# Performance work log

Measured on AMD Instinct MI355X. Metric: run time of the kernel, lower is better.

Reference implementation:

```python
import jax, jax.numpy as jnp
import numpy as np


def gcn_layer(x, W, b, src, dst):
    """PyG GCNConv with improved=True: A_hat = A + 2I, D^-1/2 A_hat D^-1/2 X W + b."""
    n = x.shape[0]
    xw = x @ W  # [N, H]
    # degree counts each incoming edge (weight 1) plus self-loop weight 2
    deg = jnp.zeros((n,), x.dtype).at[dst].add(jnp.ones((src.shape[0],), x.dtype)) + 2.0
    dinv = jax.lax.rsqrt(deg)  # deg >= 2 always
    norm = (dinv[src] * dinv[dst])[:, None]  # [E, 1]
    agg = jax.ops.segment_sum(xw[src] * norm, dst, num_segments=n)  # scatter-add to dst
    agg = agg + (2.0 * dinv * dinv)[:, None] * xw  # self-loop contribution (weight 2)
    return agg + b


def xavier(k, shape):
    lim = (6.0 / (shape[0] + shape[1])) ** 0.5
    return jax.random.uniform(k, shape, jnp.float32, -lim, lim)


def setup_inputs() -> dict:
    key = jax.random.key(0)
    ks = jax.random.split(key, 8)
    N, E, D = 100_000, 1_600_000, 64  # nodes, edges, features_dim
    H1, H2 = 64, 64                   # gnn_dims
    M1, M2 = 128, 64                  # ind_pol_dims
    rep = jax.random.normal(ks[0], (N, D), jnp.float32)
    edge_index = jax.random.randint(ks[1], (2, E), 0, N, jnp.int32)
    return {
        "rep": rep,
        "edge_index": edge_index,
        "W1": xavier(ks[2], (D, H1)), "b1": jnp.zeros((H1,), jnp.float32),
        "W2": xavier(ks[3], (H1, H2)), "b2": jnp.zeros((H2,), jnp.float32),
        "Wa": xavier(ks[4], (H2 + D, M1)), "ba": jnp.zeros((M1,), jnp.float32),
        "Wb": xavier(ks[5], (M1, M2)), "bb": jnp.zeros((M2,), jnp.float32),
        "Wo": xavier(ks[6], (M2, 1)), "bo": jnp.zeros((1,), jnp.float32),
    }


def reference(rep, edge_index, W1, b1, W2, b2, Wa, ba, Wb, bb, Wo, bo):
    src, dst = edge_index[0], edge_index[1]
    # eval mode: f.dropout(training=False) is identity
    h = jax.nn.relu(gcn_layer(rep, W1, b1, src, dst))
    h = jax.nn.relu(gcn_layer(h, W2, b2, src, dst))
    z = jnp.concatenate([rep, h], axis=1)  # [N, D + H2]
    z = jax.nn.relu(z @ Wa + ba)
    z = jax.nn.relu(z @ Wb + bb)
    prob = jax.nn.sigmoid(z @ Wo + bo)[:, 0]  # [N]
    # gumbel_softmax(hard=True, tau=1) over logits = [1-p, p] (torch semantics:
    # probabilities fed directly as logits, as in the original code)
    logits = jnp.stack([1.0 - prob, prob], axis=1)  # [N, 2]
    u = jax.random.uniform(jax.random.key(42), logits.shape, jnp.float32, 1e-20, 1.0)
    g = -jnp.log(-jnp.log(u))
    y = jax.nn.softmax(logits + g, axis=1)
    hard = jax.nn.one_hot(jnp.argmax(y, axis=1), 2, dtype=y.dtype)
    st = hard + y - jax.lax.stop_gradient(y)  # straight-through
    ind = st @ jnp.array([[0.0], [1.0]], dtype=y.dtype)  # mm with [[0],[1]]
    return (prob, ind[:, 0])
```

## Files before the change

kernel.cpp:

```cpp
#include <hip/hip_runtime.h>
#include <math.h>


__device__ __forceinline__ unsigned rotl32(unsigned x, int r) {
  return (x << r) | (x >> (32 - r));
}

__device__ __forceinline__ void threefry2x32(unsigned k0, unsigned k1,
                                             unsigned x0, unsigned x1,
                                             unsigned& o0, unsigned& o1) {
  unsigned ks2 = k0 ^ k1 ^ 0x1BD11BDAu;
#define TF_RND(r) { x0 += x1; x1 = rotl32(x1, (r)); x1 ^= x0; }
  x0 += k0; x1 += k1;
  TF_RND(13) TF_RND(15) TF_RND(26) TF_RND(6)
  x0 += k1; x1 += ks2 + 1u;
  TF_RND(17) TF_RND(29) TF_RND(16) TF_RND(24)
  x0 += ks2; x1 += k0 + 2u;
  TF_RND(13) TF_RND(15) TF_RND(26) TF_RND(6)
  x0 += k0; x1 += k1 + 3u;
  TF_RND(17) TF_RND(29) TF_RND(16) TF_RND(24)
  x0 += k1; x1 += ks2 + 4u;
  TF_RND(13) TF_RND(15) TF_RND(26) TF_RND(6)
  x0 += ks2; x1 += k0 + 5u;
#undef TF_RND
  o0 = x0; o1 = x1;
}

__device__ __forceinline__ unsigned jax_random_bits_u32(unsigned k0, unsigned k1,
                                                        unsigned flat_idx) {
  unsigned a, b;
  threefry2x32(k0, k1, 0u, flat_idx, a, b);
  return a ^ b;
}

#define BSHIFT 8
#define BMASK 255

__global__ __launch_bounds__(256) void coarse_hist_kernel(
    const int* __restrict__ dst, int* __restrict__ coarse, int E) {
  __shared__ int h[512];
  for (int i = threadIdx.x; i < 512; i += 256) h[i] = 0;
  __syncthreads();
  for (int e = blockIdx.x * blockDim.x + threadIdx.x; e < E;
       e += gridDim.x * blockDim.x)
    atomicAdd(&h[dst[e] >> BSHIFT], 1);
  __syncthreads();
  for (int i = threadIdx.x; i < 512; i += 256)
    if (h[i]) atomicAdd(&coarse[i], h[i]);
}

__global__ __launch_bounds__(512) void coarse_scan_kernel(
    const int* __restrict__ coarse, int* __restrict__ bbase,
    int* __restrict__ cbase, int NBUCK) {
  __shared__ int sh[512];
  int t = threadIdx.x;
  int v = (t < NBUCK) ? coarse[t] : 0;
  sh[t] = v;
  __syncthreads();
  for (int o = 1; o < 512; o <<= 1) {
    int a = (t >= o) ? sh[t - o] : 0;
    __syncthreads();
    sh[t] += a;
    __syncthreads();
  }
  if (t < NBUCK) {
    int ex = sh[t] - v;
    bbase[t] = ex;
    cbase[t] = ex;
    if (t == NBUCK - 1) bbase[NBUCK] = sh[t];
  }
}

#define CHUNK 4096
__global__ __launch_bounds__(256) void bucket_scatter_kernel(
    const int* __restrict__ src, const int* __restrict__ dst,
    int* __restrict__ cbase, int* __restrict__ pkB, int E) {
  __shared__ int sS[CHUNK];
  __shared__ int dS[CHUNK];
  __shared__ int cnt[512];
  __shared__ int base[512];
  const int t = threadIdx.x;
  const int e0 = blockIdx.x * CHUNK;
  const int n = min(CHUNK, E - e0);
  for (int i = t; i < 512; i += 256) cnt[i] = 0;
  for (int i = t; i < n; i += 256) {
    sS[i] = src[e0 + i];
    dS[i] = dst[e0 + i];
  }
  __syncthreads();
  for (int i = t; i < n; i += 256) atomicAdd(&cnt[dS[i] >> BSHIFT], 1);
  __syncthreads();
  for (int i = t; i < 512; i += 256) {
    int c = cnt[i];
    base[i] = c ? atomicAdd(&cbase[i], c) : 0;
  }
  __syncthreads();
  for (int i = t; i < 512; i += 256) cnt[i] = 0;
  __syncthreads();
  for (int i = t; i < n; i += 256) {
    int d = dS[i];
    int b = d >> BSHIFT;
    int r = atomicAdd(&cnt[b], 1);
    pkB[base[b] + r] = ((d & BMASK) << 20) | sS[i];
  }
}

__global__ __launch_bounds__(256) void bucket_finalize_kernel(
    const int* __restrict__ pkB, const int* __restrict__ bbase,
    int* __restrict__ off, float* __restrict__ dinv, int* __restrict__ srcS,
    int N) {
  __shared__ int cnt[256];
  __shared__ int sh[256];
  const int t = threadIdx.x;
  const int b = blockIdx.x;
  const int lo = bbase[b], hi = bbase[b + 1];
  cnt[t] = 0;
  __syncthreads();
  for (int i = lo + t; i < hi; i += 256) atomicAdd(&cnt[pkB[i] >> 20], 1);
  __syncthreads();
  const int deg = cnt[t];
  sh[t] = deg;
  __syncthreads();
  for (int o = 1; o < 256; o <<= 1) {
    int a = (t >= o) ? sh[t - o] : 0;
    __syncthreads();
    sh[t] += a;
    __syncthreads();
  }
  const int ex = sh[t] - deg;
  const int node = (b << BSHIFT) + t;
  if (node < N) {
    off[node] = lo + ex;
    dinv[node] = 1.0f / sqrtf((float)deg + 2.0f);
    if (node == N - 1) off[N] = hi;
  }
  cnt[t] = lo + ex;
  __syncthreads();
  for (int i = lo + t; i < hi; i += 256) {
    int u = pkB[i];
    int pos = atomicAdd(&cnt[u >> 20], 1);
    srcS[pos] = u & 0xFFFFF;
  }
}

__global__ __launch_bounds__(256) void aggregate_kernel(
    const float* __restrict__ xws, const int* __restrict__ srcS,
    const int* __restrict__ off, const float* __restrict__ dinv,
    const float* __restrict__ bias, float* __restrict__ h, int N) {
  int node = (blockIdx.x * blockDim.x + threadIdx.x) >> 6;
  int lane = threadIdx.x & 63;
  int g = lane >> 4;
  int fq = lane & 15;
  if (node >= N) return;
  const float4* xw4 = (const float4*)xws;
  int beg = off[node], end = off[node + 1];
  float4 a0 = make_float4(0.f, 0.f, 0.f, 0.f);
  float4 a1 = a0, a2 = a0, a3 = a0;
  for (int e = beg; e < end; e += 16) {
    int e0 = e + g, e1 = e + 4 + g, e2 = e + 8 + g, e3 = e + 12 + g;
    int s0 = srcS[min(e0, end - 1)];
    int s1 = srcS[min(e1, end - 1)];
    int s2 = srcS[min(e2, end - 1)];
    int s3 = srcS[min(e3, end - 1)];
    float4 v0 = xw4[(size_t)s0 * 16 + fq];
    float4 v1 = xw4[(size_t)s1 * 16 + fq];
    float4 v2 = xw4[(size_t)s2 * 16 + fq];
    float4 v3 = xw4[(size_t)s3 * 16 + fq];
    if (e0 < end) { a0.x += v0.x; a0.y += v0.y; a0.z += v0.z; a0.w += v0.w; }
    if (e1 < end) { a1.x += v1.x; a1.y += v1.y; a1.z += v1.z; a1.w += v1.w; }
    if (e2 < end) { a2.x += v2.x; a2.y += v2.y; a2.z += v2.z; a2.w += v2.w; }
    if (e3 < end) { a3.x += v3.x; a3.y += v3.y; a3.z += v3.z; a3.w += v3.w; }
  }
  float4 a;
  a.x = (a0.x + a1.x) + (a2.x + a3.x);
  a.y = (a0.y + a1.y) + (a2.y + a3.y);
  a.z = (a0.z + a1.z) + (a2.z + a3.z);
  a.w = (a0.w + a1.w) + (a2.w + a3.w);
  a.x += __shfl_xor(a.x, 16, 64); a.x += __shfl_xor(a.x, 32, 64);
  a.y += __shfl_xor(a.y, 16, 64); a.y += __shfl_xor(a.y, 32, 64);
  a.z += __shfl_xor(a.z, 16, 64); a.z += __shfl_xor(a.z, 32, 64);
  a.w += __shfl_xor(a.w, 16, 64); a.w += __shfl_xor(a.w, 32, 64);
  if (g == 0) {
    float di = dinv[node];
    float4 self = xw4[(size_t)node * 16 + fq];
    float4 b = ((const float4*)bias)[fq];
    float4 r;
    r.x = fmaxf(di * (a.x + 2.0f * self.x) + b.x, 0.f);
    r.y = fmaxf(di * (a.y + 2.0f * self.y) + b.y, 0.f);
    r.z = fmaxf(di * (a.z + 2.0f * self.z) + b.z, 0.f);
    r.w = fmaxf(di * (a.w + 2.0f * self.w) + b.w, 0.f);
    *(float4*)&h[(size_t)node * 64 + fq * 4] = r;
  }
}

__global__ __launch_bounds__(256) void gemm64v2_kernel(
    const float* __restrict__ X, const float* __restrict__ W,
    const float* __restrict__ dinv, float* __restrict__ Y, int N, int flags) {
  __shared__ float Ws[64 * 64];
  __shared__ float Xs[64 * 68];
  const int t = threadIdx.x;
  {
    const float4* W4 = (const float4*)W;
    float4* Ws4 = (float4*)Ws;
    for (int i = t; i < 16 * 64; i += 256) Ws4[i] = W4[i];
  }
  const int row0 = blockIdx.x * 64;
  for (int i = t; i < 64 * 16; i += 256) {
    int r = i >> 4, c4 = i & 15;
    int gr = row0 + r;
    float4 v = make_float4(0.f, 0.f, 0.f, 0.f);
    if (gr < N) v = *(const float4*)&X[(size_t)gr * 64 + c4 * 4];
    *(float4*)&Xs[r * 68 + c4 * 4] = v;
  }
  __syncthreads();

  const int tx = t & 15, ty = t >> 4;
  const int c0 = tx * 4;
  const int r0 = ty * 4;
  float acc[4][4];
#pragma unroll
  for (int i = 0; i < 4; ++i)
#pragma unroll
    for (int j = 0; j < 4; ++j) acc[i][j] = 0.f;

#pragma unroll 4
  for (int k4 = 0; k4 < 16; ++k4) {
    float4 xv[4];
#pragma unroll
    for (int i = 0; i < 4; ++i)
      xv[i] = *(const float4*)&Xs[(r0 + i) * 68 + k4 * 4];
#pragma unroll
    for (int kk = 0; kk < 4; ++kk) {
      float w[4];
#pragma unroll
      for (int j = 0; j < 4; ++j) w[j] = Ws[(k4 * 4 + kk) * 64 + c0 + j];
      const float xk[4] = {
          kk == 0 ? xv[0].x : kk == 1 ? xv[0].y : kk == 2 ? xv[0].z : xv[0].w,
          kk == 0 ? xv[1].x : kk == 1 ? xv[1].y : kk == 2 ? xv[1].z : xv[1].w,
          kk == 0 ? xv[2].x : kk == 1 ? xv[2].y : kk == 2 ? xv[2].z : xv[2].w,
          kk == 0 ? xv[3].x : kk == 1 ? xv[3].y : kk == 2 ? xv[3].z : xv[3].w};
#pragma unroll
      for (int i = 0; i < 4; ++i)
#pragma unroll
        for (int j = 0; j < 4; ++j) acc[i][j] = fmaf(xk[i], w[j], acc[i][j]);
    }
  }

#pragma unroll
  for (int i = 0; i < 4; ++i) {
    int gr = row0 + r0 + i;
    if (gr >= N) continue;
    float sc = (flags & 8) ? dinv[gr] : 1.0f;
    float4 v = make_float4(acc[i][0], acc[i][1], acc[i][2], acc[i][3]);
    if (flags & 8) { v.x *= sc; v.y *= sc; v.z *= sc; v.w *= sc; }
    *(float4*)&Y[(size_t)gr * 64 + c0] = v;
  }
}

__global__ __launch_bounds__(256) void head_mega_kernel(
    const float* __restrict__ rep, const float* __restrict__ h2,
    const float* __restrict__ Wa, const float* __restrict__ ba,
    const float* __restrict__ Wb, const float* __restrict__ bb,
    const float* __restrict__ Wo, const float* __restrict__ bo,
    float* __restrict__ out, int N) {
  __shared__ float Xs[64 * 128];
  __shared__ float Wbuf[32 * 128];
  const int t = threadIdx.x;
  const int row0 = blockIdx.x * 64;

  for (int i = t; i < 2048; i += 256) {
    int r = i >> 5, c4 = i & 31;
    int gr = row0 + r;
    float4 v = make_float4(0.f, 0.f, 0.f, 0.f);
    if (gr < N)
      v = (c4 < 16) ? *(const float4*)&rep[(size_t)gr * 64 + c4 * 4]
                    : *(const float4*)&h2[(size_t)gr * 64 + (c4 - 16) * 4];
    int scol = (c4 * 4 + ((r >> 2) << 2)) & 127;
    *(float4*)&Xs[r * 128 + scol] = v;
  }

  const int tx = t & 15, ty = t >> 4;
  const int cL = tx * 4;
  const int cH = 64 + tx * 4;
  const int r0 = ty * 4;
  float za[4][8];
#pragma unroll
  for (int i = 0; i < 4; ++i)
#pragma unroll
    for (int j = 0; j < 8; ++j) za[i][j] = 0.f;

  for (int chunk = 0; chunk < 4; ++chunk) {
    __syncthreads();
    const float4* Wa4 = (const float4*)(Wa + chunk * 32 * 128);
    float4* Wd = (float4*)Wbuf;
    for (int i = t; i < 1024; i += 256) Wd[i] = Wa4[i];
    __syncthreads();
    const int kb = chunk * 32;
#pragma unroll 2
    for (int kk = 0; kk < 32; ++kk) {
      const int kc = (kb + kk + (ty << 2)) & 127;
      float x[4];
#pragma unroll
      for (int i = 0; i < 4; ++i) x[i] = Xs[(r0 + i) * 128 + kc];
      float4 w0 = *(const float4*)&Wbuf[kk * 128 + cL];
      float4 w1 = *(const float4*)&Wbuf[kk * 128 + cH];
      const float w[8] = {w0.x, w0.y, w0.z, w0.w, w1.x, w1.y, w1.z, w1.w};
#pragma unroll
      for (int i = 0; i < 4; ++i)
#pragma unroll
        for (int j = 0; j < 8; ++j) za[i][j] = fmaf(x[i], w[j], za[i][j]);
    }
  }
#pragma unroll
  for (int i = 0; i < 4; ++i) {
#pragma unroll
    for (int j = 0; j < 4; ++j) {
      za[i][j] = fmaxf(za[i][j] + ba[cL + j], 0.f);
      za[i][4 + j] = fmaxf(za[i][4 + j] + ba[cH + j], 0.f);
    }
  }

  __syncthreads();
  float* zaS = Xs;
  {
    int sL = (cL + (ty << 2)) & 127;
    int sH = (cH + (ty << 2)) & 127;
#pragma unroll
    for (int i = 0; i < 4; ++i) {
      *(float4*)&zaS[(r0 + i) * 128 + sL] =
          make_float4(za[i][0], za[i][1], za[i][2], za[i][3]);
      *(float4*)&zaS[(r0 + i) * 128 + sH] =
          make_float4(za[i][4], za[i][5], za[i][6], za[i][7]);
    }
  }

  const int c0b = tx * 4;
  float zb[4][4];
#pragma unroll
  for (int i = 0; i < 4; ++i)
#pragma unroll
    for (int j = 0; j < 4; ++j) zb[i][j] = 0.f;

  for (int chunk = 0; chunk < 2; ++chunk) {
    __syncthreads();
    const float4* Wb4 = (const float4*)(Wb + chunk * 64 * 64);
    float4* Wd = (float4*)Wbuf;
    for (int i = t; i < 1024; i += 256) Wd[i] = Wb4[i];
    __syncthreads();
    const int kb = chunk * 64;
#pragma unroll 4
    for (int kk = 0; kk < 64; ++kk) {
      const int kc = (kb + kk + (ty << 2)) & 127;
      float x[4];
#pragma unroll
      for (int i = 0; i < 4; ++i) x[i] = zaS[(r0 + i) * 128 + kc];
      float4 w = *(const float4*)&Wbuf[kk * 64 + c0b];
      const float wj[4] = {w.x, w.y, w.z, w.w};
#pragma unroll
      for (int i = 0; i < 4; ++i)
#pragma unroll
        for (int j = 0; j < 4; ++j) zb[i][j] = fmaf(x[i], wj[j], zb[i][j]);
    }
  }
  float part[4];
#pragma unroll
  for (int i = 0; i < 4; ++i) {
    part[i] = 0.f;
#pragma unroll
    for (int j = 0; j < 4; ++j) {
      float v = fmaxf(zb[i][j] + bb[c0b + j], 0.f);
      part[i] = fmaf(v, Wo[c0b + j], part[i]);
    }
  }
  __syncthreads();
  float* red = Wbuf;
#pragma unroll
  for (int i = 0; i < 4; ++i) red[tx * 68 + r0 + i] = part[i];
  __syncthreads();
  if (t < 64) {
    int gr = row0 + t;
    if (gr < N) {
      float s = 0.f;
#pragma unroll
      for (int u = 0; u < 16; ++u) s += red[u * 68 + t];
      float w = s + bo[0];
      float p = 1.0f / (1.0f + expf(-w));
      unsigned i = (unsigned)gr;
      unsigned bits0 = jax_random_bits_u32(0u, 42u, 2u * i);
      unsigned bits1 = jax_random_bits_u32(0u, 42u, 2u * i + 1u);
      float f0 = __uint_as_float((bits0 >> 9) | 0x3f800000u) - 1.0f;
      float f1 = __uint_as_float((bits1 >> 9) | 0x3f800000u) - 1.0f;
      float u0 = fmaxf(1e-20f, f0 + 1e-20f);
      float u1 = fmaxf(1e-20f, f1 + 1e-20f);
      float g0 = -logf(-logf(u0));
      float g1 = -logf(-logf(u1));
      float a0 = (1.0f - p) + g0;
      float a1 = p + g1;
      float m = fmaxf(a0, a1);
      float e0 = expf(a0 - m), e1 = expf(a1 - m);
      float ssum = e0 + e1;
      float y0 = e0 / ssum, y1 = e1 / ssum;
      float hard1 = (y1 > y0) ? 1.0f : 0.0f;
      float st1 = (hard1 + y1) - y1;
      out[gr] = p;
      out[N + gr] = st1;
    }
  }
}

extern "C" void kernel_launch(void* const* d_in, const int* in_sizes, int n_in,
                              void* d_out, int out_size, void* d_ws, size_t ws_size,
                              hipStream_t stream) {
  const float* rep = (const float*)d_in[0];
  const int* ei = (const int*)d_in[1];
  const float* W1 = (const float*)d_in[2];
  const float* b1 = (const float*)d_in[3];
  const float* W2 = (const float*)d_in[4];
  const float* b2 = (const float*)d_in[5];
  const float* Wa = (const float*)d_in[6];
  const float* ba = (const float*)d_in[7];
  const float* Wb = (const float*)d_in[8];
  const float* bb = (const float*)d_in[9];
  const float* Wo = (const float*)d_in[10];
  const float* bo = (const float*)d_in[11];
  float* out = (float*)d_out;

  const int N = in_sizes[0] / 64;
  const int E = in_sizes[1] / 2;
  const int* srcI = ei;
  const int* dstI = ei + E;

  const int NBUCK = (N + 255) >> BSHIFT;

  float* ws = (float*)d_ws;
  float* bufA = ws;
  float* bufB = bufA + (size_t)N * 64;
  float* dinv = bufB + (size_t)N * 64;
  int* coarse = (int*)(dinv + N);
  int* bbase = coarse + 512;
  int* cbase = bbase + 513;
  int* off = cbase + 512;
  int* pkB = off + N + 1;
  int* srcS = pkB + E;

  const int nb64 = (N + 63) / 64;
  const int nbW = (N + 3) / 4;
  const int nbA = (E + CHUNK - 1) / CHUNK;

  hipMemsetAsync(coarse, 0, 512 * 4, stream);
  coarse_hist_kernel<<<256, 256, 0, stream>>>(dstI, coarse, E);
  coarse_scan_kernel<<<1, 512, 0, stream>>>(coarse, bbase, cbase, NBUCK);
  bucket_scatter_kernel<<<nbA, 256, 0, stream>>>(srcI, dstI, cbase, pkB, E);
  bucket_finalize_kernel<<<NBUCK, 256, 0, stream>>>(pkB, bbase, off, dinv,
                                                    srcS, N);

  gemm64v2_kernel<<<nb64, 256, 0, stream>>>(rep, W1, dinv, bufA, N, 8);
  aggregate_kernel<<<nbW, 256, 0, stream>>>(bufA, srcS, off, dinv, b1, bufB, N);

  gemm64v2_kernel<<<nb64, 256, 0, stream>>>(bufB, W2, dinv, bufA, N, 8);
  aggregate_kernel<<<nbW, 256, 0, stream>>>(bufA, srcS, off, dinv, b2, bufB, N);

  head_mega_kernel<<<nb64, 256, 0, stream>>>(rep, bufB, Wa, ba, Wb, bb, Wo, bo,
                                             out, N);
}
```

Measured before the change: 391.0 us.

## Fuse neighbor aggregation into following GEMM and MLP head kernels

Each aggregation is fused into its consumer. The first layer's gather now feeds a 64-row tile in shared memory that is multiplied by W2 in the same kernel, and the second layer's gather fills the h2 half of the head kernel's input tile. This removes two intermediate N×64 writes and reads and two kernel launches. The gather now runs over 64-node blocks, 16 nodes per wave, with fewer blocks in flight, which may reduce latency hiding for the irregular gathers. The head inner loops are also reworked to load float4 activations from shared memory.

```diff
diff --git a/kernel.cpp b/kernel.cpp
--- a/kernel.cpp
+++ b/kernel.cpp
@@ -143,17 +143,10 @@
   }
 }
 
-__global__ __launch_bounds__(256) void aggregate_kernel(
-    const float* __restrict__ xws, const int* __restrict__ srcS,
-    const int* __restrict__ off, const float* __restrict__ dinv,
-    const float* __restrict__ bias, float* __restrict__ h, int N) {
-  int node = (blockIdx.x * blockDim.x + threadIdx.x) >> 6;
-  int lane = threadIdx.x & 63;
-  int g = lane >> 4;
-  int fq = lane & 15;
-  if (node >= N) return;
-  const float4* xw4 = (const float4*)xws;
-  int beg = off[node], end = off[node + 1];
+__device__ __forceinline__ float4 gather_node_row(
+    const float4* __restrict__ xw4, const int* __restrict__ srcS,
+    const float* __restrict__ dinv, const float* __restrict__ bias,
+    int node, int beg, int end, int g, int fq) {
   float4 a0 = make_float4(0.f, 0.f, 0.f, 0.f);
   float4 a1 = a0, a2 = a0, a3 = a0;
   for (int e = beg; e < end; e += 16) {
@@ -180,22 +173,20 @@
   a.y += __shfl_xor(a.y, 16, 64); a.y += __shfl_xor(a.y, 32, 64);
   a.z += __shfl_xor(a.z, 16, 64); a.z += __shfl_xor(a.z, 32, 64);
   a.w += __shfl_xor(a.w, 16, 64); a.w += __shfl_xor(a.w, 32, 64);
-  if (g == 0) {
-    float di = dinv[node];
-    float4 self = xw4[(size_t)node * 16 + fq];
-    float4 b = ((const float4*)bias)[fq];
-    float4 r;
-    r.x = fmaxf(di * (a.x + 2.0f * self.x) + b.x, 0.f);
-    r.y = fmaxf(di * (a.y + 2.0f * self.y) + b.y, 0.f);
-    r.z = fmaxf(di * (a.z + 2.0f * self.z) + b.z, 0.f);
-    r.w = fmaxf(di * (a.w + 2.0f * self.w) + b.w, 0.f);
-    *(float4*)&h[(size_t)node * 64 + fq * 4] = r;
-  }
+  float di = dinv[node];
+  float4 self = xw4[(size_t)node * 16 + fq];
+  float4 b = ((const float4*)bias)[fq];
+  float4 r;
+  r.x = fmaxf(di * (a.x + 2.0f * self.x) + b.x, 0.f);
+  r.y = fmaxf(di * (a.y + 2.0f * self.y) + b.y, 0.f);
+  r.z = fmaxf(di * (a.z + 2.0f * self.z) + b.z, 0.f);
+  r.w = fmaxf(di * (a.w + 2.0f * self.w) + b.w, 0.f);
+  return r;
 }
 
 __global__ __launch_bounds__(256) void gemm64v2_kernel(
     const float* __restrict__ X, const float* __restrict__ W,
-    const float* __restrict__ dinv, float* __restrict__ Y, int N, int flags) {
+    const float* __restrict__ dinv, float* __restrict__ Y, int N) {
   __shared__ float Ws[64 * 64];
   __shared__ float Xs[64 * 68];
   const int t = threadIdx.x;
@@ -250,15 +241,87 @@
   for (int i = 0; i < 4; ++i) {
     int gr = row0 + r0 + i;
     if (gr >= N) continue;
-    float sc = (flags & 8) ? dinv[gr] : 1.0f;
-    float4 v = make_float4(acc[i][0], acc[i][1], acc[i][2], acc[i][3]);
-    if (flags & 8) { v.x *= sc; v.y *= sc; v.z *= sc; v.w *= sc; }
+    float sc = dinv[gr];
+    float4 v = make_float4(acc[i][0] * sc, acc[i][1] * sc, acc[i][2] * sc,
+                           acc[i][3] * sc);
     *(float4*)&Y[(size_t)gr * 64 + c0] = v;
   }
 }
 
-__global__ __launch_bounds__(256) void head_mega_kernel(
-    const float* __restrict__ rep, const float* __restrict__ h2,
+__global__ __launch_bounds__(256) void agg_gemm_kernel(
+    const float* __restrict__ xws, const int* __restrict__ srcS,
+    const int* __restrict__ off, const float* __restrict__ dinv,
+    const float* __restrict__ bias, const float* __restrict__ W,
+    float* __restrict__ Y, int N) {
+  __shared__ float Xs[64 * 68];
+  __shared__ float Ws[64 * 64];
+  const int t = threadIdx.x;
+  const int row0 = blockIdx.x * 64;
+  const int wave = t >> 6, lane = t & 63;
+  const int g = lane >> 4, fq = lane & 15;
+
+  {
+    const float4* W4 = (const float4*)W;
+    float4* Ws4 = (float4*)Ws;
+    for (int i = t; i < 1024; i += 256) Ws4[i] = W4[i];
+  }
+  const float4* xw4 = (const float4*)xws;
+  for (int idx = wave; idx < 64; idx += 4) {
+    int node = row0 + idx;
+    if (node >= N) continue;
+    int beg = off[node], end = off[node + 1];
+    float4 r = gather_node_row(xw4, srcS, dinv, bias, node, beg, end, g, fq);
+    if (g == 0) *(float4*)&Xs[idx * 68 + fq * 4] = r;
+  }
+  __syncthreads();
+
+  const int tx = t & 15, ty = t >> 4;
+  const int c0 = tx * 4;
+  const int r0 = ty * 4;
+  float acc[4][4];
+#pragma unroll
+  for (int i = 0; i < 4; ++i)
+#pragma unroll
+    for (int j = 0; j < 4; ++j) acc[i][j] = 0.f;
+
+#pragma unroll 4
+  for (int k4 = 0; k4 < 16; ++k4) {
+    float4 xv[4];
+#pragma unroll
+    for (int i = 0; i < 4; ++i)
+      xv[i] = *(const float4*)&Xs[(r0 + i) * 68 + k4 * 4];
+#pragma unroll
+    for (int kk = 0; kk < 4; ++kk) {
+      float w[4];
+#pragma unroll
+      for (int j = 0; j < 4; ++j) w[j] = Ws[(k4 * 4 + kk) * 64 + c0 + j];
+      const float xk[4] = {
+          kk == 0 ? xv[0].x : kk == 1 ? xv[0].y : kk == 2 ? xv[0].z : xv[0].w,
+          kk == 0 ? xv[1].x : kk == 1 ? xv[1].y : kk == 2 ? xv[1].z : xv[1].w,
+          kk == 0 ? xv[2].x : kk == 1 ? xv[2].y : kk == 2 ? xv[2].z : xv[2].w,
+          kk == 0 ? xv[3].x : kk == 1 ? xv[3].y : kk == 2 ? xv[3].z : xv[3].w};
+#pragma unroll
+      for (int i = 0; i < 4; ++i)
+#pragma unroll
+        for (int j = 0; j < 4; ++j) acc[i][j] = fmaf(xk[i], w[j], acc[i][j]);
+    }
+  }
+
+#pragma unroll
+  for (int i = 0; i < 4; ++i) {
+    int gr = row0 + r0 + i;
+    if (gr >= N) continue;
+    float sc = dinv[gr];
+    float4 v = make_float4(acc[i][0] * sc, acc[i][1] * sc, acc[i][2] * sc,
+                           acc[i][3] * sc);
+    *(float4*)&Y[(size_t)gr * 64 + c0] = v;
+  }
+}
+
+__global__ __launch_bounds__(256) void agg_head_kernel(
+    const float* __restrict__ xws2, const int* __restrict__ srcS,
+    const int* __restrict__ off, const float* __restrict__ dinv,
+    const float* __restrict__ b2, const float* __restrict__ rep,
     const float* __restrict__ Wa, const float* __restrict__ ba,
     const float* __restrict__ Wb, const float* __restrict__ bb,
     const float* __restrict__ Wo, const float* __restrict__ bo,
@@ -267,16 +330,27 @@
   __shared__ float Wbuf[32 * 128];
   const int t = threadIdx.x;
   const int row0 = blockIdx.x * 64;
-
-  for (int i = t; i < 2048; i += 256) {
-    int r = i >> 5, c4 = i & 31;
+  const int wave = t >> 6, lane = t & 63;
+  const int g = lane >> 4, fq = lane & 15;
+
+  for (int i = t; i < 1024; i += 256) {
+    int r = i >> 4, c4 = i & 15;
     int gr = row0 + r;
     float4 v = make_float4(0.f, 0.f, 0.f, 0.f);
-    if (gr < N)
-      v = (c4 < 16) ? *(const float4*)&rep[(size_t)gr * 64 + c4 * 4]
-                    : *(const float4*)&h2[(size_t)gr * 64 + (c4 - 16) * 4];
+    if (gr < N) v = *(const float4*)&rep[(size_t)gr * 64 + c4 * 4];
     int scol = (c4 * 4 + ((r >> 2) << 2)) & 127;
     *(float4*)&Xs[r * 128 + scol] = v;
+  }
+  const float4* xw4 = (const float4*)xws2;
+  for (int idx = wave; idx < 64; idx += 4) {
+    int node = row0 + idx;
+    if (node >= N) continue;
+    int beg = off[node], end = off[node + 1];
+    float4 r = gather_node_row(xw4, srcS, dinv, b2, node, beg, end, g, fq);
+    if (g == 0) {
+      int scol = ((64 + fq * 4) + ((idx >> 2) << 2)) & 127;
+      *(float4*)&Xs[idx * 128 + scol] = r;
+    }
   }
 
   const int tx = t & 15, ty = t >> 4;
@@ -296,19 +370,26 @@
     for (int i = t; i < 1024; i += 256) Wd[i] = Wa4[i];
     __syncthreads();
     const int kb = chunk * 32;
-#pragma unroll 2
-    for (int kk = 0; kk < 32; ++kk) {
-      const int kc = (kb + kk + (ty << 2)) & 127;
-      float x[4];
-#pragma unroll
-      for (int i = 0; i < 4; ++i) x[i] = Xs[(r0 + i) * 128 + kc];
-      float4 w0 = *(const float4*)&Wbuf[kk * 128 + cL];
-      float4 w1 = *(const float4*)&Wbuf[kk * 128 + cH];
-      const float w[8] = {w0.x, w0.y, w0.z, w0.w, w1.x, w1.y, w1.z, w1.w};
+    for (int k4 = 0; k4 < 8; ++k4) {
+      const int kc = (kb + k4 * 4 + (ty << 2)) & 127;
+      float4 xq[4];
 #pragma unroll
       for (int i = 0; i < 4; ++i)
-#pragma unroll
-        for (int j = 0; j < 8; ++j) za[i][j] = fmaf(x[i], w[j], za[i][j]);
+        xq[i] = *(const float4*)&Xs[(r0 + i) * 128 + kc];
+#pragma unroll
+      for (int sub = 0; sub < 4; ++sub) {
+        const int kk = k4 * 4 + sub;
+        float4 w0 = *(const float4*)&Wbuf[kk * 128 + cL];
+        float4 w1 = *(const float4*)&Wbuf[kk * 128 + cH];
+        const float w[8] = {w0.x, w0.y, w0.z, w0.w, w1.x, w1.y, w1.z, w1.w};
+#pragma unroll
+        for (int i = 0; i < 4; ++i) {
+          float x = sub == 0 ? xq[i].x : sub == 1 ? xq[i].y
+                  : sub == 2 ? xq[i].z : xq[i].w;
+#pragma unroll
+          for (int j = 0; j < 8; ++j) za[i][j] = fmaf(x, w[j], za[i][j]);
+        }
+      }
     }
   }
 #pragma unroll
@@ -348,18 +429,25 @@
     for (int i = t; i < 1024; i += 256) Wd[i] = Wb4[i];
     __syncthreads();
     const int kb = chunk * 64;
-#pragma unroll 4
-    for (int kk = 0; kk < 64; ++kk) {
-      const int kc = (kb + kk + (ty << 2)) & 127;
-      float x[4];
-#pragma unroll
-      for (int i = 0; i < 4; ++i) x[i] = zaS[(r0 + i) * 128 + kc];
-      float4 w = *(const float4*)&Wbuf[kk * 64 + c0b];
-      const float wj[4] = {w.x, w.y, w.z, w.w};
+    for (int k4 = 0; k4 < 16; ++k4) {
+      const int kc = (kb + k4 * 4 + (ty << 2)) & 127;
+      float4 xq[4];
 #pragma unroll
       for (int i = 0; i < 4; ++i)
-#pragma unroll
-        for (int j = 0; j < 4; ++j) zb[i][j] = fmaf(x[i], wj[j], zb[i][j]);
+        xq[i] = *(const float4*)&zaS[(r0 + i) * 128 + kc];
+#pragma unroll
+      for (int sub = 0; sub < 4; ++sub) {
+        const int kk = k4 * 4 + sub;
+        float4 w = *(const float4*)&Wbuf[kk * 64 + c0b];
+        const float wj[4] = {w.x, w.y, w.z, w.w};
+#pragma unroll
+        for (int i = 0; i < 4; ++i) {
+          float x = sub == 0 ? xq[i].x : sub == 1 ? xq[i].y
+                  : sub == 2 ? xq[i].z : xq[i].w;
+#pragma unroll
+          for (int j = 0; j < 4; ++j) zb[i][j] = fmaf(x, wj[j], zb[i][j]);
+        }
+      }
     }
   }
   float part[4];
@@ -444,7 +532,6 @@
   int* srcS = pkB + E;
 
   const int nb64 = (N + 63) / 64;
-  const int nbW = (N + 3) / 4;
   const int nbA = (E + CHUNK - 1) / CHUNK;
 
   hipMemsetAsync(coarse, 0, 512 * 4, stream);
@@ -454,12 +541,11 @@
   bucket_finalize_kernel<<<NBUCK, 256, 0, stream>>>(pkB, bbase, off, dinv,
                                                     srcS, N);
 
-  gemm64v2_kernel<<<nb64, 256, 0, stream>>>(rep, W1, dinv, bufA, N, 8);
-  aggregate_kernel<<<nbW, 256, 0, stream>>>(bufA, srcS, off, dinv, b1, bufB, N);
-
-  gemm64v2_kernel<<<nb64, 256, 0, stream>>>(bufB, W2, dinv, bufA, N, 8);
-  aggregate_kernel<<<nbW, 256, 0, stream>>>(bufA, srcS, off, dinv, b2, bufB, N);
-
-  head_mega_kernel<<<nb64, 256, 0, stream>>>(rep, bufB, Wa, ba, Wb, bb, Wo, bo,
-                                             out, N);
-}
+  gemm64v2_kernel<<<nb64, 256, 0, stream>>>(rep, W1, dinv, bufA, N);
+
+  agg_gemm_kernel<<<nb64, 256, 0, stream>>>(bufA, srcS, off, dinv, b1, W2,
+                                            bufB, N);
+
+  agg_head_kernel<<<nb64, 256, 0, stream>>>(bufB, srcS, off, dinv, b2, rep,
+                                            Wa, ba, Wb, bb, Wo, bo, out, N);
+}
```

Result: slower. 533.3 us (+36.4%).

## Fuse first GEMM into bucket scatter launch, apply source dinv in aggregation

Applied to the files above, without the earlier changes.

The first X@W1 GEMM no longer depends on dinv, so it now runs as extra blocks of the bucket scatter kernel and overlaps with the edge sort. Because of that, the layer-1 aggregation multiplies each gathered neighbour row by dinv[src] and scales the self term by dinv itself. This removes one kernel launch and its serialization. In exchange, layer 1 does an extra scalar gather per edge, and the merged kernel carries larger shared memory and extra branches.

```diff
diff --git a/kernel.cpp b/kernel.cpp
--- a/kernel.cpp
+++ b/kernel.cpp
@@ -72,36 +72,100 @@
 }
 
 #define CHUNK 4096
-__global__ __launch_bounds__(256) void bucket_scatter_kernel(
+__global__ __launch_bounds__(256) void scatter_gemm_kernel(
     const int* __restrict__ src, const int* __restrict__ dst,
-    int* __restrict__ cbase, int* __restrict__ pkB, int E) {
-  __shared__ int sS[CHUNK];
-  __shared__ int dS[CHUNK];
-  __shared__ int cnt[512];
-  __shared__ int base[512];
+    int* __restrict__ cbase, int* __restrict__ pkB, int E, int nbA,
+    const float* __restrict__ X, const float* __restrict__ W,
+    float* __restrict__ Y, int N) {
+  __shared__ int smem[9216];
   const int t = threadIdx.x;
-  const int e0 = blockIdx.x * CHUNK;
-  const int n = min(CHUNK, E - e0);
-  for (int i = t; i < 512; i += 256) cnt[i] = 0;
-  for (int i = t; i < n; i += 256) {
-    sS[i] = src[e0 + i];
-    dS[i] = dst[e0 + i];
-  }
-  __syncthreads();
-  for (int i = t; i < n; i += 256) atomicAdd(&cnt[dS[i] >> BSHIFT], 1);
-  __syncthreads();
-  for (int i = t; i < 512; i += 256) {
-    int c = cnt[i];
-    base[i] = c ? atomicAdd(&cbase[i], c) : 0;
-  }
-  __syncthreads();
-  for (int i = t; i < 512; i += 256) cnt[i] = 0;
-  __syncthreads();
-  for (int i = t; i < n; i += 256) {
-    int d = dS[i];
-    int b = d >> BSHIFT;
-    int r = atomicAdd(&cnt[b], 1);
-    pkB[base[b] + r] = ((d & BMASK) << 20) | sS[i];
+
+  if (blockIdx.x < nbA) {
+    int* sS = smem;
+    int* dS = smem + 4096;
+    int* cnt = smem + 8192;
+    int* base = smem + 8704;
+    const int e0 = blockIdx.x * CHUNK;
+    const int n = min(CHUNK, E - e0);
+    for (int i = t; i < 512; i += 256) cnt[i] = 0;
+    for (int i = t; i < n; i += 256) {
+      sS[i] = src[e0 + i];
+      dS[i] = dst[e0 + i];
+    }
+    __syncthreads();
+    for (int i = t; i < n; i += 256) atomicAdd(&cnt[dS[i] >> BSHIFT], 1);
+    __syncthreads();
+    for (int i = t; i < 512; i += 256) {
+      int c = cnt[i];
+      base[i] = c ? atomicAdd(&cbase[i], c) : 0;
+    }
+    __syncthreads();
+    for (int i = t; i < 512; i += 256) cnt[i] = 0;
+    __syncthreads();
+    for (int i = t; i < n; i += 256) {
+      int d = dS[i];
+      int b = d >> BSHIFT;
+      int r = atomicAdd(&cnt[b], 1);
+      pkB[base[b] + r] = ((d & BMASK) << 20) | sS[i];
+    }
+    return;
+  }
+
+  float* Ws = (float*)smem;
+  float* Xs = (float*)smem + 4096;
+  {
+    const float4* W4 = (const float4*)W;
+    float4* Ws4 = (float4*)Ws;
+    for (int i = t; i < 1024; i += 256) Ws4[i] = W4[i];
+  }
+  const int row0 = (blockIdx.x - nbA) * 64;
+  for (int i = t; i < 64 * 16; i += 256) {
+    int r = i >> 4, c4 = i & 15;
+    int gr = row0 + r;
+    float4 v = make_float4(0.f, 0.f, 0.f, 0.f);
+    if (gr < N) v = *(const float4*)&X[(size_t)gr * 64 + c4 * 4];
+    *(float4*)&Xs[r * 68 + c4 * 4] = v;
+  }
+  __syncthreads();
+
+  const int tx = t & 15, ty = t >> 4;
+  const int c0 = tx * 4;
+  const int r0 = ty * 4;
+  float acc[4][4];
+#pragma unroll
+  for (int i = 0; i < 4; ++i)
+#pragma unroll
+    for (int j = 0; j < 4; ++j) acc[i][j] = 0.f;
+
+#pragma unroll 4
+  for (int k4 = 0; k4 < 16; ++k4) {
+    float4 xv[4];
+#pragma unroll
+    for (int i = 0; i < 4; ++i)
+      xv[i] = *(const float4*)&Xs[(r0 + i) * 68 + k4 * 4];
+#pragma unroll
+    for (int kk = 0; kk < 4; ++kk) {
+      float w[4];
+#pragma unroll
+      for (int j = 0; j < 4; ++j) w[j] = Ws[(k4 * 4 + kk) * 64 + c0 + j];
+      const float xk[4] = {
+          kk == 0 ? xv[0].x : kk == 1 ? xv[0].y : kk == 2 ? xv[0].z : xv[0].w,
+          kk == 0 ? xv[1].x : kk == 1 ? xv[1].y : kk == 2 ? xv[1].z : xv[1].w,
+          kk == 0 ? xv[2].x : kk == 1 ? xv[2].y : kk == 2 ? xv[2].z : xv[2].w,
+          kk == 0 ? xv[3].x : kk == 1 ? xv[3].y : kk == 2 ? xv[3].z : xv[3].w};
+#pragma unroll
+      for (int i = 0; i < 4; ++i)
+#pragma unroll
+        for (int j = 0; j < 4; ++j) acc[i][j] = fmaf(xk[i], w[j], acc[i][j]);
+    }
+  }
+
+#pragma unroll
+  for (int i = 0; i < 4; ++i) {
+    int gr = row0 + r0 + i;
+    if (gr >= N) continue;
+    float4 v = make_float4(acc[i][0], acc[i][1], acc[i][2], acc[i][3]);
+    *(float4*)&Y[(size_t)gr * 64 + c0] = v;
   }
 }
 
@@ -146,7 +210,8 @@
 __global__ __launch_bounds__(256) void aggregate_kernel(
     const float* __restrict__ xws, const int* __restrict__ srcS,
     const int* __restrict__ off, const float* __restrict__ dinv,
-    const float* __restrict__ bias, float* __restrict__ h, int N) {
+    const float* __restrict__ dinvS, const float* __restrict__ bias,
+    float* __restrict__ h, int N) {
   int node = (blockIdx.x * blockDim.x + threadIdx.x) >> 6;
   int lane = threadIdx.x & 63;
   int g = lane >> 4;
@@ -156,20 +221,39 @@
   int beg = off[node], end = off[node + 1];
   float4 a0 = make_float4(0.f, 0.f, 0.f, 0.f);
   float4 a1 = a0, a2 = a0, a3 = a0;
-  for (int e = beg; e < end; e += 16) {
-    int e0 = e + g, e1 = e + 4 + g, e2 = e + 8 + g, e3 = e + 12 + g;
-    int s0 = srcS[min(e0, end - 1)];
-    int s1 = srcS[min(e1, end - 1)];
-    int s2 = srcS[min(e2, end - 1)];
-    int s3 = srcS[min(e3, end - 1)];
-    float4 v0 = xw4[(size_t)s0 * 16 + fq];
-    float4 v1 = xw4[(size_t)s1 * 16 + fq];
-    float4 v2 = xw4[(size_t)s2 * 16 + fq];
-    float4 v3 = xw4[(size_t)s3 * 16 + fq];
-    if (e0 < end) { a0.x += v0.x; a0.y += v0.y; a0.z += v0.z; a0.w += v0.w; }
-    if (e1 < end) { a1.x += v1.x; a1.y += v1.y; a1.z += v1.z; a1.w += v1.w; }
-    if (e2 < end) { a2.x += v2.x; a2.y += v2.y; a2.z += v2.z; a2.w += v2.w; }
-    if (e3 < end) { a3.x += v3.x; a3.y += v3.y; a3.z += v3.z; a3.w += v3.w; }
+  if (dinvS) {
+    for (int e = beg; e < end; e += 16) {
+      int e0 = e + g, e1 = e + 4 + g, e2 = e + 8 + g, e3 = e + 12 + g;
+      int s0 = srcS[min(e0, end - 1)];
+      int s1 = srcS[min(e1, end - 1)];
+      int s2 = srcS[min(e2, end - 1)];
+      int s3 = srcS[min(e3, end - 1)];
+      float d0 = dinvS[s0], d1 = dinvS[s1], d2 = dinvS[s2], d3 = dinvS[s3];
+      float4 v0 = xw4[(size_t)s0 * 16 + fq];
+      float4 v1 = xw4[(size_t)s1 * 16 + fq];
+      float4 v2 = xw4[(size_t)s2 * 16 + fq];
+      float4 v3 = xw4[(size_t)s3 * 16 + fq];
+      if (e0 < end) { a0.x += d0*v0.x; a0.y += d0*v0.y; a0.z += d0*v0.z; a0.w += d0*v0.w; }
+      if (e1 < end) { a1.x += d1*v1.x; a1.y += d1*v1.y; a1.z += d1*v1.z; a1.w += d1*v1.w; }
+      if (e2 < end) { a2.x += d2*v2.x; a2.y += d2*v2.y; a2.z += d2*v2.z; a2.w += d2*v2.w; }
+      if (e3 < end) { a3.x += d3*v3.x; a3.y += d3*v3.y; a3.z += d3*v3.z; a3.w += d3*v3.w; }
+    }
+  } else {
+    for (int e = beg; e < end; e += 16) {
+      int e0 = e + g, e1 = e + 4 + g, e2 = e + 8 + g, e3 = e + 12 + g;
+      int s0 = srcS[min(e0, end - 1)];
+      int s1 = srcS[min(e1, end - 1)];
+      int s2 = srcS[min(e2, end - 1)];
+      int s3 = srcS[min(e3, end - 1)];
+      float4 v0 = xw4[(size_t)s0 * 16 + fq];
+      float4 v1 = xw4[(size_t)s1 * 16 + fq];
+      float4 v2 = xw4[(size_t)s2 * 16 + fq];
+      float4 v3 = xw4[(size_t)s3 * 16 + fq];
+      if (e0 < end) { a0.x += v0.x; a0.y += v0.y; a0.z += v0.z; a0.w += v0.w; }
+      if (e1 < end) { a1.x += v1.x; a1.y += v1.y; a1.z += v1.z; a1.w += v1.w; }
+      if (e2 < end) { a2.x += v2.x; a2.y += v2.y; a2.z += v2.z; a2.w += v2.w; }
+      if (e3 < end) { a3.x += v3.x; a3.y += v3.y; a3.z += v3.z; a3.w += v3.w; }
+    }
   }
   float4 a;
   a.x = (a0.x + a1.x) + (a2.x + a3.x);
@@ -183,6 +267,7 @@
   if (g == 0) {
     float di = dinv[node];
     float4 self = xw4[(size_t)node * 16 + fq];
+    if (dinvS) { self.x *= di; self.y *= di; self.z *= di; self.w *= di; }
     float4 b = ((const float4*)bias)[fq];
     float4 r;
     r.x = fmaxf(di * (a.x + 2.0f * self.x) + b.x, 0.f);
@@ -195,7 +280,7 @@
 
 __global__ __launch_bounds__(256) void gemm64v2_kernel(
     const float* __restrict__ X, const float* __restrict__ W,
-    const float* __restrict__ dinv, float* __restrict__ Y, int N, int flags) {
+    const float* __restrict__ dinv, float* __restrict__ Y, int N) {
   __shared__ float Ws[64 * 64];
   __shared__ float Xs[64 * 68];
   const int t = threadIdx.x;
@@ -250,9 +335,9 @@
   for (int i = 0; i < 4; ++i) {
     int gr = row0 + r0 + i;
     if (gr >= N) continue;
-    float sc = (flags & 8) ? dinv[gr] : 1.0f;
-    float4 v = make_float4(acc[i][0], acc[i][1], acc[i][2], acc[i][3]);
-    if (flags & 8) { v.x *= sc; v.y *= sc; v.z *= sc; v.w *= sc; }
+    float sc = dinv[gr];
+    float4 v = make_float4(acc[i][0] * sc, acc[i][1] * sc, acc[i][2] * sc,
+                           acc[i][3] * sc);
     *(float4*)&Y[(size_t)gr * 64 + c0] = v;
   }
 }
@@ -450,15 +535,17 @@
   hipMemsetAsync(coarse, 0, 512 * 4, stream);
   coarse_hist_kernel<<<256, 256, 0, stream>>>(dstI, coarse, E);
   coarse_scan_kernel<<<1, 512, 0, stream>>>(coarse, bbase, cbase, NBUCK);
-  bucket_scatter_kernel<<<nbA, 256, 0, stream>>>(srcI, dstI, cbase, pkB, E);
+  scatter_gemm_kernel<<<nbA + nb64, 256, 0, stream>>>(
+      srcI, dstI, cbase, pkB, E, nbA, rep, W1, bufA, N);
   bucket_finalize_kernel<<<NBUCK, 256, 0, stream>>>(pkB, bbase, off, dinv,
                                                     srcS, N);
 
-  gemm64v2_kernel<<<nb64, 256, 0, stream>>>(rep, W1, dinv, bufA, N, 8);
-  aggregate_kernel<<<nbW, 256, 0, stream>>>(bufA, srcS, off, dinv, b1, bufB, N);
-
-  gemm64v2_kernel<<<nb64, 256, 0, stream>>>(bufB, W2, dinv, bufA, N, 8);
-  aggregate_kernel<<<nbW, 256, 0, stream>>>(bufA, srcS, off, dinv, b2, bufB, N);
+  aggregate_kernel<<<nbW, 256, 0, stream>>>(bufA, srcS, off, dinv, dinv, b1,
+                                            bufB, N);
+
+  gemm64v2_kernel<<<nb64, 256, 0, stream>>>(bufB, W2, dinv, bufA, N);
+  aggregate_kernel<<<nbW, 256, 0, stream>>>(bufA, srcS, off, dinv, nullptr, b2,
+                                            bufB, N);
 
   head_mega_kernel<<<nb64, 256, 0, stream>>>(rep, bufB, Wa, ba, Wb, bb, Wo, bo,
                                              out, N);
```

Result: no change. 387.1 us (-1.0%).
